# Kernel tuning notes

Hardware: AMD Instinct MI355X
Metric: run time of the kernel (lower is better)

The kernel has to match this reference:

```python
import jax, jax.numpy as jnp
import numpy as np

SCALING = 32.0 / 16.0  # alpha / rank


def setup_inputs() -> dict:
    key = jax.random.key(0)
    k_x, k_w, k_a, k_b, k_m = jax.random.split(key, 5)
    B, S, D_IN, D_OUT, R = 4, 8192, 1024, 1024, 16
    x = jax.random.normal(k_x, (B, S, D_IN), dtype=jnp.float32)
    weight = jax.random.normal(k_w, (D_OUT, D_IN), dtype=jnp.float32) * (1.0 / np.sqrt(D_IN))
    a_w = jax.random.normal(k_a, (R, D_IN), dtype=jnp.float32) * (1.0 / np.sqrt(D_IN))
    b_w = jax.random.normal(k_b, (D_OUT, R), dtype=jnp.float32) * (1.0 / np.sqrt(R))
    magnitude = jax.random.uniform(k_m, (1, D_OUT), dtype=jnp.float32) + 0.5
    return {"x": x, "weight": weight, "a_w": a_w, "b_w": b_w, "magnitude": magnitude}


def reference(x, weight, a_w, b_w, magnitude):
    # Base linear: x @ W^T  -> [B, S, out_dim]
    base_out = jnp.einsum('bsd,od->bso', x, weight)
    # LoRA adapter: scaling * B(A(x)) (dropout p=0 -> identity)
    lora_out = SCALING * jnp.einsum('bsr,or->bso', jnp.einsum('bsd,rd->bsr', x, a_w), b_w)
    # DoRA: reconstruct effective weight, row-norm over in_dim (dim=1)
    w_eff = weight + SCALING * (b_w @ a_w)            # [out_dim, in_dim]
    weight_norm = jnp.linalg.norm(w_eff, axis=1)      # [out_dim] (detached in torch)
    mag_norm_scale = (magnitude / weight_norm).reshape(1, 1, -1)  # broadcast over [B,S,out]
    dora_out = (mag_norm_scale - 1.0) * base_out + mag_norm_scale * lora_out
    # LoRALinear.forward returns base_out + lora branch output
    return base_out + dora_out
```

## Files before the change

### kernel.cpp

```cpp
#include <hip/hip_runtime.h>
#include <hip/hip_bf16.h>


typedef __bf16 bf16x8 __attribute__((ext_vector_type(8)));
typedef __bf16 bf16x4 __attribute__((ext_vector_type(4)));
typedef float  f32x4  __attribute__((ext_vector_type(4)));

#define D_IN  1024
#define D_OUT 1024
#define M_TOT 32768
#define BM 128
#define BN 128
#define BK 32
#define LDS_STRIDE 56

__global__ void dora_prep(const float* __restrict__ w,
                          const float* __restrict__ a_w,
                          const float* __restrict__ b_w,
                          const float* __restrict__ mag,
                          __bf16* __restrict__ wb,
                          float* __restrict__ scale) {
    const int o = blockIdx.x;
    const int t = threadIdx.x;

    float bw[16];
#pragma unroll
    for (int r = 0; r < 16; ++r) bw[r] = b_w[o * 16 + r];

    float ss = 0.f;
#pragma unroll
    for (int i = 0; i < 4; ++i) {
        const int k = t + i * 256;
        float dot = 0.f;
#pragma unroll
        for (int r = 0; r < 16; ++r) dot = fmaf(bw[r], a_w[r * D_IN + k], dot);
        const float acc = fmaf(2.0f, dot, w[o * D_IN + k]);
        wb[o * D_IN + k] = (__bf16)acc;
        ss = fmaf(acc, acc, ss);
    }
#pragma unroll
    for (int off = 32; off; off >>= 1) ss += __shfl_down(ss, off, 64);
    __shared__ float wsum[4];
    if ((t & 63) == 0) wsum[t >> 6] = ss;
    __syncthreads();
    if (t == 0) {
        const float tot = wsum[0] + wsum[1] + wsum[2] + wsum[3];
        scale[o] = mag[o] / sqrtf(tot);
    }
}

__global__ void dora_gemm(const float* __restrict__ x,
                          const __bf16* __restrict__ wb,
                          const float* __restrict__ scale,
                          float* __restrict__ out) {
    __shared__ __bf16 As[BM][LDS_STRIDE];
    __shared__ __bf16 Bs[BN][LDS_STRIDE];

    const int bx = blockIdx.x;
    const int bn = (bx & 7) * BN;
    const int bm = (bx >> 3) * BM;
    const int t  = threadIdx.x;
    const int lane = t & 63;
    const int wave = t >> 6;
    const int wm = (wave & 1) * 64;
    const int wn = (wave >> 1) * 64;
    const int lm = lane & 15;
    const int lq = lane >> 4;

    f32x4 acc[4][4] = {};

    const float* xbase = x + (size_t)bm * D_IN;
    const __bf16* wbase = wb + (size_t)bn * D_IN;

    for (int kk = 0; kk < D_IN; kk += BK) {
#pragma unroll
        for (int j = 0; j < 4; ++j) {
            const int r = j * 32 + (t >> 3);
            const int k = (t & 7) * 4;
            const float4 v = *(const float4*)(xbase + (size_t)r * D_IN + kk + k);
            bf16x4 p = { (__bf16)v.x, (__bf16)v.y, (__bf16)v.z, (__bf16)v.w };
            *(bf16x4*)(&As[r][k]) = p;
        }
#pragma unroll
        for (int j = 0; j < 2; ++j) {
            const int n = j * 64 + (t >> 2);
            const int k = (t & 3) * 8;
            bf16x8 v = *(const bf16x8*)(wbase + (size_t)n * D_IN + kk + k);
            *(bf16x8*)(&Bs[n][k]) = v;
        }
        __syncthreads();

        bf16x8 af[4], bfr[4];
#pragma unroll
        for (int i = 0; i < 4; ++i)
            af[i] = *(const bf16x8*)(&As[wm + i * 16 + lm][lq * 8]);
#pragma unroll
        for (int i = 0; i < 4; ++i)
            bfr[i] = *(const bf16x8*)(&Bs[wn + i * 16 + lm][lq * 8]);

#pragma unroll
        for (int i = 0; i < 4; ++i)
#pragma unroll
            for (int j = 0; j < 4; ++j)
                acc[i][j] = __builtin_amdgcn_mfma_f32_16x16x32_bf16(af[i], bfr[j], acc[i][j], 0, 0, 0);
        __syncthreads();
    }

#pragma unroll
    for (int j = 0; j < 4; ++j) {
        const int n = bn + wn + j * 16 + lm;
        const float sc = scale[n];
#pragma unroll
        for (int i = 0; i < 4; ++i) {
            const int m = bm + wm + i * 16 + lq * 4;
#pragma unroll
            for (int r = 0; r < 4; ++r) {
                out[(size_t)(m + r) * D_OUT + n] = acc[i][j][r] * sc;
            }
        }
    }
}

extern "C" void kernel_launch(void* const* d_in, const int* in_sizes, int n_in,
                              void* d_out, int out_size, void* d_ws, size_t ws_size,
                              hipStream_t stream) {
    const float* x    = (const float*)d_in[0];
    const float* w    = (const float*)d_in[1];
    const float* a_w  = (const float*)d_in[2];
    const float* b_w  = (const float*)d_in[3];
    const float* mag  = (const float*)d_in[4];
    float* out = (float*)d_out;

    __bf16* wb   = (__bf16*)d_ws;
    float* scale = (float*)((char*)d_ws + (size_t)D_OUT * D_IN * sizeof(__bf16));

    dora_prep<<<D_OUT, 256, 0, stream>>>(w, a_w, b_w, mag, wb, scale);

    const int grid = (M_TOT / BM) * (D_OUT / BN);
    dora_gemm<<<grid, 256, 0, stream>>>(x, wb, scale, out);
}
```

Baseline: 357.1 us.

## Pre-convert x to bf16 and load GEMM tiles via direct global-to-LDS

Adds a separate pass that converts x to bf16 once, so the GEMM no longer reloads and converts fp32 x eight times (once per N tile). Tile staging now uses global_load_lds 16-byte direct transfers instead of a register round trip, and the padded LDS layout becomes unpadded. The cost is an extra kernel that reads 128MB and writes 64MB. The unpadded layout risks LDS bank conflicts on fragment reads, and there is still no double buffering.

```diff
diff --git a/kernel.cpp b/kernel.cpp
--- a/kernel.cpp
+++ b/kernel.cpp
@@ -12,7 +12,22 @@
 #define BM 128
 #define BN 128
 #define BK 32
-#define LDS_STRIDE 56
+
+__device__ __forceinline__ void gl_lds16(const __bf16* g, __bf16* l) {
+    __builtin_amdgcn_global_load_lds(
+        (const __attribute__((address_space(1))) void*)g,
+        (__attribute__((address_space(3))) void*)l,
+        16, 0, 0);
+}
+
+__global__ void x_to_bf16(const float* __restrict__ x, __bf16* __restrict__ xb) {
+    const size_t idx = ((size_t)blockIdx.x * blockDim.x + threadIdx.x) * 8;
+    const float4 v0 = *(const float4*)(x + idx);
+    const float4 v1 = *(const float4*)(x + idx + 4);
+    bf16x8 p = { (__bf16)v0.x, (__bf16)v0.y, (__bf16)v0.z, (__bf16)v0.w,
+                 (__bf16)v1.x, (__bf16)v1.y, (__bf16)v1.z, (__bf16)v1.w };
+    *(bf16x8*)(xb + idx) = p;
+}
 
 __global__ void dora_prep(const float* __restrict__ w,
                           const float* __restrict__ a_w,
@@ -49,12 +64,12 @@
     }
 }
 
-__global__ void dora_gemm(const float* __restrict__ x,
+__global__ void dora_gemm(const __bf16* __restrict__ xb,
                           const __bf16* __restrict__ wb,
                           const float* __restrict__ scale,
                           float* __restrict__ out) {
-    __shared__ __bf16 As[BM][LDS_STRIDE];
-    __shared__ __bf16 Bs[BN][LDS_STRIDE];
+    __shared__ __bf16 As[BM * BK];
+    __shared__ __bf16 Bs[BN * BK];
 
     const int bx = blockIdx.x;
     const int bn = (bx & 7) * BN;
@@ -69,34 +84,31 @@
 
     f32x4 acc[4][4] = {};
 
-    const float* xbase = x + (size_t)bm * D_IN;
-    const __bf16* wbase = wb + (size_t)bn * D_IN;
+    const int srow0 = wave * 32 + (lane >> 2);
+    const int scol  = (lane & 3) * 8;
+    const __bf16* ag0 = xb + (size_t)(bm + srow0) * D_IN + scol;
+    const __bf16* ag1 = ag0 + 16 * D_IN;
+    const __bf16* bg0 = wb + (size_t)(bn + srow0) * D_IN + scol;
+    const __bf16* bg1 = bg0 + 16 * D_IN;
+    __bf16* al0 = As + wave * 1024;
+    __bf16* al1 = As + wave * 1024 + 512;
+    __bf16* bl0 = Bs + wave * 1024;
+    __bf16* bl1 = Bs + wave * 1024 + 512;
 
     for (int kk = 0; kk < D_IN; kk += BK) {
-#pragma unroll
-        for (int j = 0; j < 4; ++j) {
-            const int r = j * 32 + (t >> 3);
-            const int k = (t & 7) * 4;
-            const float4 v = *(const float4*)(xbase + (size_t)r * D_IN + kk + k);
-            bf16x4 p = { (__bf16)v.x, (__bf16)v.y, (__bf16)v.z, (__bf16)v.w };
-            *(bf16x4*)(&As[r][k]) = p;
-        }
-#pragma unroll
-        for (int j = 0; j < 2; ++j) {
-            const int n = j * 64 + (t >> 2);
-            const int k = (t & 3) * 8;
-            bf16x8 v = *(const bf16x8*)(wbase + (size_t)n * D_IN + kk + k);
-            *(bf16x8*)(&Bs[n][k]) = v;
-        }
+        gl_lds16(ag0 + kk, al0);
+        gl_lds16(ag1 + kk, al1);
+        gl_lds16(bg0 + kk, bl0);
+        gl_lds16(bg1 + kk, bl1);
         __syncthreads();
 
         bf16x8 af[4], bfr[4];
 #pragma unroll
         for (int i = 0; i < 4; ++i)
-            af[i] = *(const bf16x8*)(&As[wm + i * 16 + lm][lq * 8]);
+            af[i] = *(const bf16x8*)(&As[(wm + i * 16 + lm) * BK + lq * 8]);
 #pragma unroll
         for (int i = 0; i < 4; ++i)
-            bfr[i] = *(const bf16x8*)(&Bs[wn + i * 16 + lm][lq * 8]);
+            bfr[i] = *(const bf16x8*)(&Bs[(wn + i * 16 + lm) * BK + lq * 8]);
 
 #pragma unroll
         for (int i = 0; i < 4; ++i)
@@ -131,11 +143,13 @@
     const float* mag  = (const float*)d_in[4];
     float* out = (float*)d_out;
 
-    __bf16* wb   = (__bf16*)d_ws;
-    float* scale = (float*)((char*)d_ws + (size_t)D_OUT * D_IN * sizeof(__bf16));
+    __bf16* xb   = (__bf16*)d_ws;
+    __bf16* wb   = (__bf16*)((char*)d_ws + (size_t)M_TOT * D_IN * 2);
+    float* scale = (float*)((char*)wb + (size_t)D_OUT * D_IN * 2);
 
+    x_to_bf16<<<(M_TOT * D_IN) / (256 * 8), 256, 0, stream>>>(x, xb);
     dora_prep<<<D_OUT, 256, 0, stream>>>(w, a_w, b_w, mag, wb, scale);
 
     const int grid = (M_TOT / BM) * (D_OUT / BN);
-    dora_gemm<<<grid, 256, 0, stream>>>(x, wb, scale, out);
+    dora_gemm<<<grid, 256, 0, stream>>>(xb, wb, scale, out);
 }
```

New measurement: 333.7 us. -6.6%, faster.
